# Kernel tuning notes

Measured on AMD Instinct MI355X. Metric: run time of the kernel, lower is better.

Reference implementation:

```python
import jax, jax.numpy as jnp
import numpy as np


def setup_inputs() -> dict:
    key = jax.random.key(0)
    kq, kk, kv, kmask = jax.random.split(key, 4)
    B, H, L, D = 2, 16, 2048, 64
    q = jax.random.normal(kq, (B, H, L, D), dtype=jnp.float32)
    k = jax.random.normal(kk, (B, H, L, D), dtype=jnp.float32)
    v = jax.random.normal(kv, (B, H, L, D), dtype=jnp.float32)
    valid = jax.random.randint(kmask, (B, H, L, L), 0, 2, dtype=jnp.int32)
    scale = jnp.ones((), dtype=jnp.float32)  # typically 1/sqrt(D)
    return {"q": q, "k": k, "v": v, "valid": valid, "scale": scale}


def reference(q, k, v, valid, scale):
    # scores: [B, H, Lq, Lk]
    att_v = jnp.einsum('bhqd,bhkd->bhqk', q, k)
    att_v = att_v * scale
    att_v = att_v - jnp.max(att_v, axis=-1, keepdims=True)
    att_v = jnp.where(valid <= 0, -jnp.inf, att_v)
    att_w = jax.nn.softmax(att_v, axis=-1)
    # rows that are fully masked produce NaN -> zero them (matches torch masked_fill on isnan)
    att_w = jnp.where(jnp.isnan(att_w), jnp.zeros((), dtype=att_w.dtype), att_w)
    result = jnp.einsum('bhqk,bhkd->bhqd', att_w, v)
    return (result, att_w)
```

## Files before the change

kernel.cpp:

```cpp
#include <hip/hip_runtime.h>
#include <hip/hip_bf16.h>
#include <hip/hip_fp16.h>

#define L_    2048
#define D_    64
#define QT    64
#define NKT   32
#define KGPITCH 260
#define VTP   72
#define PBP   72

typedef _Float16 half8 __attribute__((ext_vector_type(8)));
typedef _Float16 half2v __attribute__((ext_vector_type(2)));
typedef float    f32x4 __attribute__((ext_vector_type(4)));

__device__ __forceinline__ f32x4 mfma16f(half8 a, half8 b, f32x4 c) {
    return __builtin_amdgcn_mfma_f32_16x16x32_f16(a, b, c, 0, 0, 0);
}

__global__ __launch_bounds__(256, 4)
void attn_fused(const float* __restrict__ Qg, const float* __restrict__ Kg,
                const float* __restrict__ Vg, const int* __restrict__ validg,
                const float* __restrict__ scaleg,
                float* __restrict__ outR, float* __restrict__ outW)
{
    __shared__ __attribute__((aligned(16))) float    Klds[16 * KGPITCH];
    __shared__ __attribute__((aligned(16))) _Float16 Vt[64 * VTP];
    __shared__ __attribute__((aligned(16))) _Float16 Pbuf[64 * PBP];

    const int tid  = threadIdx.x;
    const int wv   = tid >> 6;
    const int lane = tid & 63;
    const int ln   = lane & 15;
    const int qd   = lane >> 4;

    const int bidx = blockIdx.x;
    const int bh   = (bidx & 7) * 4 + ((bidx >> 3) & 3);
    const int qt   = bidx >> 5;

    const float scale = scaleg[0];

    const float* Qb = Qg + ((size_t)bh * L_ + (size_t)qt * QT) * D_;
    const float* Kb = Kg + (size_t)bh * L_ * D_;
    const float* Vb = Vg + (size_t)bh * L_ * D_;
    const int*   Mb = validg + ((size_t)bh * L_ + (size_t)qt * QT) * (size_t)L_;
    float* Ob = outR + ((size_t)bh * L_ + (size_t)qt * QT) * D_;
    float* Wb = outW + ((size_t)bh * L_ + (size_t)qt * QT) * (size_t)L_;

    half8 aF[2];
    {
        const float* qrow = Qb + (size_t)(wv * 16 + ln) * D_;
#pragma unroll
        for (int f = 0; f < 2; ++f) {
            f32x4 x0 = *(const f32x4*)(qrow + f * 32 + qd * 8);
            f32x4 x1 = *(const f32x4*)(qrow + f * 32 + qd * 8 + 4);
            half8 h;
#pragma unroll
            for (int j = 0; j < 4; ++j) { h[j] = (_Float16)x0[j]; h[4 + j] = (_Float16)x1[j]; }
            aF[f] = h;
        }
    }

    auto stageK = [&](int kt) {
        const float* gbase = Kb + (size_t)kt * 64 * 64;
#pragma unroll
        for (int gi = 0; gi < 4; ++gi) {
            const int grp = wv * 4 + gi;
            __builtin_amdgcn_global_load_lds(
                (const __attribute__((address_space(1))) void*)(gbase + grp * 256 + lane * 4),
                (__attribute__((address_space(3))) void*)&Klds[grp * KGPITCH],
                16, 0, 0);
        }
    };

    auto kfrags = [&](int kr, half8& b0, half8& b1) {
        const float* kp = &Klds[(kr >> 2) * KGPITCH + (kr & 3) * 64 + qd * 8];
        f32x4 x0 = *(const f32x4*)kp;
        f32x4 x1 = *(const f32x4*)(kp + 4);
        f32x4 y0 = *(const f32x4*)(kp + 32);
        f32x4 y1 = *(const f32x4*)(kp + 36);
#pragma unroll
        for (int j = 0; j < 4; ++j) {
            b0[j] = (_Float16)x0[j]; b0[4 + j] = (_Float16)x1[j];
            b1[j] = (_Float16)y0[j]; b1[4 + j] = (_Float16)y1[j];
        }
    };

    const int* maskbase = Mb + (size_t)(wv * 16 + qd * 4) * L_ + ln;

    unsigned mreg[16];
#pragma unroll
    for (int i = 0; i < 16; ++i) mreg[i] = 0u;
    float lsum[4] = {0.f, 0.f, 0.f, 0.f};

    for (int kt = 0; kt < NKT; ++kt) {
        __syncthreads();
        stageK(kt);
        int mv[16];
#pragma unroll
        for (int ct = 0; ct < 4; ++ct)
#pragma unroll
            for (int r = 0; r < 4; ++r)
                mv[ct * 4 + r] = maskbase[(size_t)r * L_ + kt * 64 + ct * 16];
        __syncthreads();
        unsigned bits = 0;
#pragma unroll
        for (int ct = 0; ct < 4; ++ct) {
            half8 b0, b1;
            kfrags(ct * 16 + ln, b0, b1);
            f32x4 acc = {0.f, 0.f, 0.f, 0.f};
            acc = mfma16f(aF[0], b0, acc);
            acc = mfma16f(aF[1], b1, acc);
#pragma unroll
            for (int r = 0; r < 4; ++r) {
                unsigned bit = (mv[ct * 4 + r] > 0) ? 1u : 0u;
                bits |= bit << (ct * 4 + r);
                lsum[r] += (float)bit * __expf(acc[r] * scale);
            }
        }
        mreg[kt >> 1] |= bits << ((kt & 1) * 16);
    }

    float invl[4];
#pragma unroll
    for (int r = 0; r < 4; ++r) {
        float v = lsum[r];
        v += __shfl_xor(v, 1);
        v += __shfl_xor(v, 2);
        v += __shfl_xor(v, 4);
        v += __shfl_xor(v, 8);
        invl[r] = v > 0.f ? 1.f / v : 0.f;
    }

    f32x4 accO[4];
#pragma unroll
    for (int i = 0; i < 4; ++i) accO[i] = (f32x4){0.f, 0.f, 0.f, 0.f};

    const int rp = tid >> 3;
    const int vc = tid & 7;
    const int dc = vc * 8;

    for (int kt = 0; kt < NKT; ++kt) {
        __syncthreads();
        stageK(kt);
        {
            const float* v0p = Vb + ((size_t)kt * 64 + 2 * rp) * 64 + dc;
            f32x4 va0 = *(const f32x4*)v0p;
            f32x4 va1 = *(const f32x4*)(v0p + 4);
            f32x4 vb0 = *(const f32x4*)(v0p + 64);
            f32x4 vb1 = *(const f32x4*)(v0p + 68);
            const int g = (rp >> 2) ^ vc;
#pragma unroll
            for (int i = 0; i < 8; ++i) {
                float f0 = (i < 4) ? va0[i] : va1[i - 4];
                float f1 = (i < 4) ? vb0[i] : vb1[i - 4];
                half2v h; h[0] = (_Float16)f0; h[1] = (_Float16)f1;
                const int d = dc + i;
                *(half2v*)&Vt[d * VTP + 8 * g + 2 * (rp & 3)] = h;
            }
        }
        __syncthreads();
#pragma unroll
        for (int ct = 0; ct < 4; ++ct) {
            half8 b0, b1;
            kfrags(ct * 16 + ln, b0, b1);
            f32x4 acc = {0.f, 0.f, 0.f, 0.f};
            acc = mfma16f(aF[0], b0, acc);
            acc = mfma16f(aF[1], b1, acc);
#pragma unroll
            for (int r = 0; r < 4; ++r) {
                const int qrow = wv * 16 + qd * 4 + r;
                float bit = (float)((mreg[kt >> 1] >> ((kt & 1) * 16 + ct * 4 + r)) & 1u);
                float p = bit * __expf(acc[r] * scale) * invl[r];
                Pbuf[qrow * PBP + ct * 16 + ln] = (_Float16)p;
            }
        }
        half8 p0 = *(const half8*)&Pbuf[(wv * 16 + ln) * PBP + qd * 8];
        half8 p1 = *(const half8*)&Pbuf[(wv * 16 + ln) * PBP + 32 + qd * 8];
        {
            float* wp = Wb + (size_t)(wv * 16 + ln) * L_ + kt * 64;
            f32x4 s0, s1, s2, s3;
#pragma unroll
            for (int j = 0; j < 4; ++j) {
                s0[j] = (float)p0[j];     s1[j] = (float)p0[4 + j];
                s2[j] = (float)p1[j];     s3[j] = (float)p1[4 + j];
            }
            *(f32x4*)(wp + qd * 8)      = s0;
            *(f32x4*)(wp + qd * 8 + 4)  = s1;
            *(f32x4*)(wp + 32 + qd * 8)     = s2;
            *(f32x4*)(wp + 32 + qd * 8 + 4) = s3;
        }
#pragma unroll
        for (int c2 = 0; c2 < 4; ++c2) {
            const int d  = c2 * 16 + ln;
            const int g2 = (d >> 3) & 7;
            half8 v0 = *(const half8*)&Vt[d * VTP + 8 * (qd ^ g2)];
            half8 v1 = *(const half8*)&Vt[d * VTP + 8 * ((4 + qd) ^ g2)];
            accO[c2] = mfma16f(p0, v0, accO[c2]);
            accO[c2] = mfma16f(p1, v1, accO[c2]);
        }
    }

#pragma unroll
    for (int c2 = 0; c2 < 4; ++c2)
#pragma unroll
        for (int r = 0; r < 4; ++r)
            Ob[(size_t)(wv * 16 + qd * 4 + r) * D_ + (c2 * 16 + ln)] = accO[c2][r];
}

extern "C" void kernel_launch(void* const* d_in, const int* in_sizes, int n_in,
                              void* d_out, int out_size, void* d_ws, size_t ws_size,
                              hipStream_t stream) {
    const float* q     = (const float*)d_in[0];
    const float* k     = (const float*)d_in[1];
    const float* v     = (const float*)d_in[2];
    const int*   valid = (const int*)d_in[3];
    const float* scale = (const float*)d_in[4];

    float* out_res  = (float*)d_out;
    float* out_attw = out_res + (size_t)2 * 16 * L_ * D_;

    dim3 grid(2 * 16 * (L_ / QT));
    dim3 block(256);
    attn_fused<<<grid, block, 0, stream>>>(q, k, v, valid, scale, out_res, out_attw);
}
```

Before: 1.121 ms.

## Register-prefetch K/V/mask tiles, store K as fp16 in LDS, spill mask bits to output

Replaces the async global-to-LDS fp32 K staging with register prefetch of the next K (and V, mask) tile. The tile is converted to fp16 once when written to LDS, so the per-fragment fp32-to-fp16 conversion on every LDS read goes away. Mask bits are packed per tile and parked in the output buffer (Ob) between the two passes instead of in registers. The aim is to overlap global loads with compute and to cut LDS traffic and register pressure, at the cost of extra global traffic for the bit slab and reliance on the later O writes overwriting it.

```diff
diff --git a/kernel.cpp b/kernel.cpp
--- a/kernel.cpp
+++ b/kernel.cpp
@@ -1,22 +1,26 @@
 #include <hip/hip_runtime.h>
-#include <hip/hip_bf16.h>
 #include <hip/hip_fp16.h>
 
 #define L_    2048
 #define D_    64
 #define QT    64
 #define NKT   32
-#define KGPITCH 260
+#define KP16  72
 #define VTP   72
 #define PBP   72
 
-typedef _Float16 half8 __attribute__((ext_vector_type(8)));
+typedef _Float16 half8  __attribute__((ext_vector_type(8)));
+typedef _Float16 half4  __attribute__((ext_vector_type(4)));
 typedef _Float16 half2v __attribute__((ext_vector_type(2)));
-typedef float    f32x4 __attribute__((ext_vector_type(4)));
+typedef float    f32x4  __attribute__((ext_vector_type(4)));
 
 __device__ __forceinline__ f32x4 mfma16f(half8 a, half8 b, f32x4 c) {
     return __builtin_amdgcn_mfma_f32_16x16x32_f16(a, b, c, 0, 0, 0);
 }
+
+#define FENCE_BAR() do { asm volatile("s_waitcnt lgkmcnt(0)" ::: "memory"); \
+                         __builtin_amdgcn_s_barrier();                       \
+                         asm volatile("" ::: "memory"); } while (0)
 
 __global__ __launch_bounds__(256, 4)
 void attn_fused(const float* __restrict__ Qg, const float* __restrict__ Kg,
@@ -24,7 +28,7 @@
                 const float* __restrict__ scaleg,
                 float* __restrict__ outR, float* __restrict__ outW)
 {
-    __shared__ __attribute__((aligned(16))) float    Klds[16 * KGPITCH];
+    __shared__ __attribute__((aligned(16))) _Float16 Klds[64 * KP16];
     __shared__ __attribute__((aligned(16))) _Float16 Vt[64 * VTP];
     __shared__ __attribute__((aligned(16))) _Float16 Pbuf[64 * PBP];
 
@@ -61,49 +65,78 @@
         }
     }
 
-    auto stageK = [&](int kt) {
-        const float* gbase = Kb + (size_t)kt * 64 * 64;
-#pragma unroll
-        for (int gi = 0; gi < 4; ++gi) {
-            const int grp = wv * 4 + gi;
-            __builtin_amdgcn_global_load_lds(
-                (const __attribute__((address_space(1))) void*)(gbase + grp * 256 + lane * 4),
-                (__attribute__((address_space(3))) void*)&Klds[grp * KGPITCH],
-                16, 0, 0);
-        }
-    };
-
-    auto kfrags = [&](int kr, half8& b0, half8& b1) {
-        const float* kp = &Klds[(kr >> 2) * KGPITCH + (kr & 3) * 64 + qd * 8];
-        f32x4 x0 = *(const f32x4*)kp;
-        f32x4 x1 = *(const f32x4*)(kp + 4);
-        f32x4 y0 = *(const f32x4*)(kp + 32);
-        f32x4 y1 = *(const f32x4*)(kp + 36);
+    f32x4 kreg[4];
+    const int kt4 = tid >> 4;
+    const int kc4 = (tid & 15) * 4;
+    auto loadK = [&](int kt) {
+        const float* base = Kb + (size_t)kt * (64 * 64);
+#pragma unroll
+        for (int j = 0; j < 4; ++j)
+            kreg[j] = *(const f32x4*)(base + (size_t)(j * 256 + tid) * 4);
+    };
+    auto writeK = [&]() {
 #pragma unroll
         for (int j = 0; j < 4; ++j) {
-            b0[j] = (_Float16)x0[j]; b0[4 + j] = (_Float16)x1[j];
-            b1[j] = (_Float16)y0[j]; b1[4 + j] = (_Float16)y1[j];
-        }
-    };
-
+            const int row = j * 16 + kt4;
+            half4 h;
+#pragma unroll
+            for (int e = 0; e < 4; ++e) h[e] = (_Float16)kreg[j][e];
+            *(half4*)&Klds[row * KP16 + kc4] = h;
+        }
+    };
+
+    f32x4 vreg[4];
+    const int rp = tid >> 3;
+    const int vc = tid & 7;
+    const int dc = vc * 8;
+    auto loadV = [&](int kt) {
+        const float* v0p = Vb + ((size_t)kt * 64 + 2 * rp) * 64 + dc;
+        vreg[0] = *(const f32x4*)v0p;
+        vreg[1] = *(const f32x4*)(v0p + 4);
+        vreg[2] = *(const f32x4*)(v0p + 64);
+        vreg[3] = *(const f32x4*)(v0p + 68);
+    };
+    auto writeV = [&]() {
+        const int g = (rp >> 2) ^ vc;
+#pragma unroll
+        for (int i = 0; i < 8; ++i) {
+            float f0 = (i < 4) ? vreg[0][i] : vreg[1][i - 4];
+            float f1 = (i < 4) ? vreg[2][i] : vreg[3][i - 4];
+            half2v h; h[0] = (_Float16)f0; h[1] = (_Float16)f1;
+            const int d = dc + i;
+            *(half2v*)&Vt[d * VTP + 8 * g + 2 * (rp & 3)] = h;
+        }
+    };
+
+    int mv[16];
     const int* maskbase = Mb + (size_t)(wv * 16 + qd * 4) * L_ + ln;
-
-    unsigned mreg[16];
-#pragma unroll
-    for (int i = 0; i < 16; ++i) mreg[i] = 0u;
-    float lsum[4] = {0.f, 0.f, 0.f, 0.f};
-
-    for (int kt = 0; kt < NKT; ++kt) {
-        __syncthreads();
-        stageK(kt);
-        int mv[16];
+    auto loadM = [&](int kt) {
 #pragma unroll
         for (int ct = 0; ct < 4; ++ct)
 #pragma unroll
             for (int r = 0; r < 4; ++r)
                 mv[ct * 4 + r] = maskbase[(size_t)r * L_ + kt * 64 + ct * 16];
-        __syncthreads();
+    };
+
+    auto kfrags = [&](int kr, half8& b0, half8& b1) {
+        const _Float16* kp = &Klds[kr * KP16 + qd * 8];
+        b0 = *(const half8*)kp;
+        b1 = *(const half8*)(kp + 32);
+    };
+
+    unsigned short* bitsSlab = (unsigned short*)Ob;
+
+    float lsum[4] = {0.f, 0.f, 0.f, 0.f};
+    loadK(0); loadM(0);
+    for (int kt = 0; kt < NKT; ++kt) {
+        FENCE_BAR();
+        writeK();
         unsigned bits = 0;
+#pragma unroll
+        for (int i = 0; i < 16; ++i) bits |= (mv[i] > 0 ? 1u : 0u) << i;
+        if (kt + 1 < NKT) { loadK(kt + 1); loadM(kt + 1); }
+        FENCE_BAR();
+        bitsSlab[kt * 256 + tid] = (unsigned short)bits;
 #pragma unroll
         for (int ct = 0; ct < 4; ++ct) {
             half8 b0, b1;
@@ -113,12 +146,10 @@
             acc = mfma16f(aF[1], b1, acc);
 #pragma unroll
             for (int r = 0; r < 4; ++r) {
-                unsigned bit = (mv[ct * 4 + r] > 0) ? 1u : 0u;
-                bits |= bit << (ct * 4 + r);
-                lsum[r] += (float)bit * __expf(acc[r] * scale);
+                float bit = (float)((bits >> (ct * 4 + r)) & 1u);
+                lsum[r] += bit * __expf(acc[r] * scale);
             }
         }
-        mreg[kt >> 1] |= bits << ((kt & 1) * 16);
     }
 
     float invl[4];
@@ -132,34 +163,25 @@
         invl[r] = v > 0.f ? 1.f / v : 0.f;
     }
 
+    asm volatile("s_waitcnt vmcnt(0)" ::: "memory");
+
     f32x4 accO[4];
 #pragma unroll
     for (int i = 0; i < 4; ++i) accO[i] = (f32x4){0.f, 0.f, 0.f, 0.f};
 
-    const int rp = tid >> 3;
-    const int vc = tid & 7;
-    const int dc = vc * 8;
-
+    loadK(0); loadV(0);
+    unsigned bcur = bitsSlab[tid];
     for (int kt = 0; kt < NKT; ++kt) {
-        __syncthreads();
-        stageK(kt);
-        {
-            const float* v0p = Vb + ((size_t)kt * 64 + 2 * rp) * 64 + dc;
-            f32x4 va0 = *(const f32x4*)v0p;
-            f32x4 va1 = *(const f32x4*)(v0p + 4);
-            f32x4 vb0 = *(const f32x4*)(v0p + 64);
-            f32x4 vb1 = *(const f32x4*)(v0p + 68);
-            const int g = (rp >> 2) ^ vc;
-#pragma unroll
-            for (int i = 0; i < 8; ++i) {
-                float f0 = (i < 4) ? va0[i] : va1[i - 4];
-                float f1 = (i < 4) ? vb0[i] : vb1[i - 4];
-                half2v h; h[0] = (_Float16)f0; h[1] = (_Float16)f1;
-                const int d = dc + i;
-                *(half2v*)&Vt[d * VTP + 8 * g + 2 * (rp & 3)] = h;
-            }
-        }
-        __syncthreads();
+        FENCE_BAR();
+        writeK();
+        writeV();
+        unsigned bnext = 0;
+        if (kt + 1 < NKT) {
+            loadK(kt + 1); loadV(kt + 1);
+            bnext = bitsSlab[(kt + 1) * 256 + tid];
+        }
+        FENCE_BAR();
+        const unsigned bits = bcur;
 #pragma unroll
         for (int ct = 0; ct < 4; ++ct) {
             half8 b0, b1;
@@ -170,7 +192,7 @@
 #pragma unroll
             for (int r = 0; r < 4; ++r) {
                 const int qrow = wv * 16 + qd * 4 + r;
-                float bit = (float)((mreg[kt >> 1] >> ((kt & 1) * 16 + ct * 4 + r)) & 1u);
+                float bit = (float)((bits >> (ct * 4 + r)) & 1u);
                 float p = bit * __expf(acc[r] * scale) * invl[r];
                 Pbuf[qrow * PBP + ct * 16 + ln] = (_Float16)p;
             }
@@ -185,8 +207,8 @@
                 s0[j] = (float)p0[j];     s1[j] = (float)p0[4 + j];
                 s2[j] = (float)p1[j];     s3[j] = (float)p1[4 + j];
             }
-            *(f32x4*)(wp + qd * 8)      = s0;
-            *(f32x4*)(wp + qd * 8 + 4)  = s1;
+            *(f32x4*)(wp + qd * 8)          = s0;
+            *(f32x4*)(wp + qd * 8 + 4)      = s1;
             *(f32x4*)(wp + 32 + qd * 8)     = s2;
             *(f32x4*)(wp + 32 + qd * 8 + 4) = s3;
         }
@@ -199,6 +221,7 @@
             accO[c2] = mfma16f(p0, v0, accO[c2]);
             accO[c2] = mfma16f(p1, v1, accO[c2]);
         }
+        bcur = bnext;
     }
 
 #pragma unroll
```

New measurement: 1.095 ms. -2.3%, faster.
